# Optimization experiments

Measured on AMD Instinct MI355X. Metric: run time of the kernel, lower is better.

The kernel has to match this reference:

```python
import jax, jax.numpy as jnp
import numpy as np

B = 65536   # batch
HS = 8      # max hand size
E = 12      # card embed dim
A = 20      # max actions
KC = 4      # max cards per action (padded with 0)
NH, HD = 4, 3  # MHA heads, head dim (12/4)


def _xavier(k, out_dim, in_dim, gain):
    lim = gain * np.sqrt(6.0 / (in_dim + out_dim))
    return jax.random.uniform(k, (out_dim, in_dim), jnp.float32, -lim, lim)


def setup_inputs() -> dict:
    key = jax.random.key(0)
    ks = jax.random.split(key, 32)
    card_emb = 0.1 * jax.random.normal(ks[0], (54, E), jnp.float32)
    card_emb = card_emb.at[0].set(0.0)  # padding_idx=0
    enemy_emb = 0.1 * jax.random.normal(ks[1], (54, E), jnp.float32)
    enemy_emb = enemy_emb.at[0].set(0.0)
    inp = {
        'hand_cards': jax.random.randint(ks[2], (B, HS), 0, 54),
        'game_state': jax.random.normal(ks[3], (B, 12), jnp.float32),
        'discard_pile_cards': jax.random.uniform(ks[4], (B, 54), jnp.float32),
        'enemy_card': jax.random.randint(ks[5], (B, 1), 0, 54),
        'hand_size': jax.random.randint(ks[6], (B,), 1, HS + 1),
        'action_card_indices': jax.random.randint(ks[7], (A, KC), 0, 54),
        'num_valid_actions': 20,
        'card_emb': card_emb,
        'enemy_emb': enemy_emb,
        'in_w': _xavier(ks[8], 3 * E, E, 0.5),   # MHA in_proj (torch layout [3E,E])
        'in_b': jnp.zeros((3 * E,), jnp.float32),
        'out_w': _xavier(ks[9], E, E, 0.5),
        'out_b': jnp.zeros((E,), jnp.float32),
        'gs_w1': _xavier(ks[10], 64, 12, 0.8), 'gs_b1': jnp.zeros((64,)),
        'gs_w2': _xavier(ks[11], 6, 64, 0.8), 'gs_b2': jnp.zeros((6,)),
        'dp_w1': _xavier(ks[12], 64, 54, 0.8), 'dp_b1': jnp.zeros((64,)),
        'dp_w2': _xavier(ks[13], 6, 64, 0.8), 'dp_b2': jnp.zeros((6,)),
        'ctx_w1': _xavier(ks[14], 128, 36, 0.8), 'ctx_b1': jnp.zeros((128,)),
        'ctx_w2': _xavier(ks[15], 128, 128, 0.8), 'ctx_b2': jnp.zeros((128,)),
        'sc_w1': _xavier(ks[16], 32, 140, 0.8), 'sc_b1': jnp.zeros((32,)),
        'sc_w2': _xavier(ks[17], 1, 32, 0.8), 'sc_b2': jnp.zeros((1,)),
    }
    return inp


def reference(hand_cards, game_state, discard_pile_cards, enemy_card, hand_size,
              action_card_indices, num_valid_actions,
              card_emb, enemy_emb, in_w, in_b, out_w, out_b,
              gs_w1, gs_b1, gs_w2, gs_b2, dp_w1, dp_b1, dp_w2, dp_b2,
              ctx_w1, ctx_b1, ctx_w2, ctx_b2, sc_w1, sc_b1, sc_w2, sc_b2):
    b = hand_cards.shape[0]
    # hand embeddings + self-attention with key padding mask (card 0 = pad)
    he = card_emb[hand_cards]                                  # [B,8,12]
    mask = hand_cards != 0                                     # [B,8]
    qkv = he @ in_w.T + in_b                                   # [B,8,36]
    q, k, v = jnp.split(qkv, 3, axis=-1)
    hsplit = lambda t: t.reshape(b, HS, NH, HD)
    s = jnp.einsum('bqhd,bkhd->bhqk', hsplit(q), hsplit(k)) / np.sqrt(HD)
    s = jnp.where(mask[:, None, None, :], s, -1e9)
    attn = jax.nn.softmax(s, axis=-1)
    att = jnp.einsum('bhqk,bkhd->bqhd', attn, hsplit(v)).reshape(b, HS, E)
    att = att @ out_w.T + out_b                                # [B,8,12]
    lengths = jnp.maximum(hand_size.astype(jnp.float32), 1.0)[:, None]
    hand_ctx = att.sum(axis=1) / lengths                       # [B,12]
    # enemy / game-state / discard encoders (eval mode: dropout off)
    en = enemy_emb[enemy_card[:, 0]]                           # [B,12]
    g = jax.nn.relu(game_state @ gs_w1.T + gs_b1) @ gs_w2.T + gs_b2        # [B,6]
    d = jax.nn.relu(discard_pile_cards @ dp_w1.T + dp_b1) @ dp_w2.T + dp_b2  # [B,6]
    ctx = jnp.concatenate([hand_ctx, en, g, d], axis=-1)       # [B,36]
    ctx = jax.nn.relu(ctx @ ctx_w1.T + ctx_b1) @ ctx_w2.T + ctx_b2         # [B,128]
    # ragged per-action card lists: masked mean of card embeddings
    aemb = card_emb[action_card_indices]                       # [A,K,12]
    am = (action_card_indices != 0).astype(jnp.float32)[..., None]
    cnt = jnp.maximum(am.sum(axis=1), 1.0)
    arep = (aemb * am).sum(axis=1) / cnt                       # [A,12]
    feat = jnp.concatenate([
        jnp.broadcast_to(ctx[:, None, :], (b, A, ctx.shape[-1])),
        jnp.broadcast_to(arep[None], (b, A, E)),
    ], axis=-1)                                                # [B,A,140]
    sc = (jax.nn.relu(feat @ sc_w1.T + sc_b1) @ sc_w2.T + sc_b2)[..., 0]   # [B,A]
    valid = jnp.arange(A) < num_valid_actions
    return jnp.where(valid[None, :], sc, -1e8)
```

## Files before the change

kernel.cpp:

```cpp
#include <hip/hip_runtime.h>
#include <math.h>

#define HS 8
#define E 12
#define NA 20
#define KC 4

typedef float f32x4 __attribute__((ext_vector_type(4)));
typedef short short8 __attribute__((ext_vector_type(8)));

__device__ float g_QKVT[54 * 48];
__device__ float g_abias[NA * 32];
__device__ __align__(16) short g_dpB[2 * 4 * 64 * 16];
__device__ __align__(16) short g_ctxB[2 * 8 * 64 * 16];
__device__ __align__(16) short g_WtB[4 * 2 * 64 * 16];

__device__ __forceinline__ void split_bf16(float f, short& hi, short& lo) {
    unsigned u = __float_as_uint(f);
    unsigned r = (u + 0x7FFFu + ((u >> 16) & 1u)) >> 16;
    hi = (short)r;
    float fh = __uint_as_float(r << 16);
    unsigned v = __float_as_uint(f - fh);
    unsigned r2 = (v + 0x7FFFu + ((v >> 16) & 1u)) >> 16;
    lo = (short)r2;
}

__global__ void precompute_kernel(const float* __restrict__ card_emb,
                                  const int* __restrict__ aci,
                                  const float* __restrict__ ctx_w2,
                                  const float* __restrict__ ctx_b2,
                                  const float* __restrict__ sc_w1,
                                  const float* __restrict__ sc_b1,
                                  const float* __restrict__ in_w,
                                  const float* __restrict__ in_b,
                                  const float* __restrict__ ctx_w1,
                                  const float* __restrict__ dp_w1) {
    int t = blockIdx.x * 256 + threadIdx.x;
    if (t < 640) {
        int a = t >> 5, j = t & 31;
        float arep[E];
#pragma unroll
        for (int k2 = 0; k2 < E; ++k2) arep[k2] = 0.f;
        float cnt = 0.f;
#pragma unroll
        for (int c = 0; c < KC; ++c) {
            int idx = aci[a * KC + c];
            if (idx != 0) {
                cnt += 1.f;
#pragma unroll
                for (int k2 = 0; k2 < E; ++k2) arep[k2] += card_emb[idx * E + k2];
            }
        }
        float inv = 1.f / fmaxf(cnt, 1.f);
        float s = sc_b1[j];
#pragma unroll
        for (int k2 = 0; k2 < E; ++k2) s += sc_w1[j * 140 + 128 + k2] * (arep[k2] * inv);
        for (int i = 0; i < 128; ++i) s += sc_w1[j * 140 + i] * ctx_b2[i];
        g_abias[t] = s;
    } else if (t < 3232) {
        int t2 = t - 640;
        int c = t2 / 48, col = t2 % 48;
        int h = col / 12, s = col % 12;
        float val = 0.f;
        if (s < 9) {
            int r;
            if (s < 3) r = h * 3 + s;
            else if (s < 6) r = 12 + h * 3 + (s - 3);
            else r = 24 + h * 3 + (s - 6);
            val = in_b[r];
#pragma unroll
            for (int j = 0; j < 12; ++j) val += in_w[r * 12 + j] * card_emb[c * 12 + j];
        }
        g_QKVT[t2] = val;
    } else if (t < 7328) {
        int id = t - 3232;
        int st = id >> 9, lane = (id >> 3) & 63, j = id & 7;
        int s = st >> 2, tt = st & 3;
        int g = lane >> 4, n = lane & 15;
        int k = 32 * s + 8 * g + j, col = 16 * tt + n;
        float w = (k < 54) ? dp_w1[col * 54 + k] : 0.f;
        short hi, lo;
        split_bf16(w, hi, lo);
        int base = ((st << 6) + lane) << 4;
        g_dpB[base + j] = hi;
        g_dpB[base + 8 + j] = lo;
    } else if (t < 15520) {
        int id = t - 7328;
        int st = id >> 9, lane = (id >> 3) & 63, j = id & 7;
        int s = st >> 3, tt = st & 7;
        int g = lane >> 4, n = lane & 15;
        int k = 32 * s + 8 * g + j, col = 16 * tt + n;
        float w = (k < 36) ? ctx_w1[col * 36 + k] : 0.f;
        short hi, lo;
        split_bf16(w, hi, lo);
        int base = ((st << 6) + lane) << 4;
        g_ctxB[base + j] = hi;
        g_ctxB[base + 8 + j] = lo;
    } else if (t < 19616) {
        int id = t - 15520;
        int st = id >> 9, lane = (id >> 3) & 63, j = id & 7;
        int s = st >> 1, tt = st & 1;
        int g = lane >> 4, n = lane & 15;
        int k = 32 * s + 8 * g + j, col = 16 * tt + n;
        float w = 0.f;
        for (int i = 0; i < 128; ++i) w += sc_w1[col * 140 + i] * ctx_w2[i * 128 + k];
        short hi, lo;
        split_bf16(w, hi, lo);
        int base = ((st << 6) + lane) << 4;
        g_WtB[base + j] = hi;
        g_WtB[base + 8 + j] = lo;
    }
}

#define MFMA(a, b, c) __builtin_amdgcn_mfma_f32_16x16x32_bf16(a, b, c, 0, 0, 0)

__global__ __launch_bounds__(256) void policy_kernel(
    const int* __restrict__ hand_cards, const float* __restrict__ game_state,
    const float* __restrict__ discard, const int* __restrict__ enemy_card,
    const int* __restrict__ hand_size, const int* __restrict__ num_valid,
    const float* __restrict__ enemy_emb, const float* __restrict__ out_w,
    const float* __restrict__ out_b, const float* __restrict__ gs_w1,
    const float* __restrict__ gs_b1, const float* __restrict__ gs_w2,
    const float* __restrict__ gs_b2, const float* __restrict__ dp_w2,
    const float* __restrict__ dp_b1, const float* __restrict__ dp_b2,
    const float* __restrict__ ctx_b1, const float* __restrict__ sc_w2,
    const float* __restrict__ sc_b2, float* __restrict__ out) {
    __shared__ __align__(16) float sS[64 * 68];
    __shared__ __align__(16) float sT[4 * 16 * 36];
    __shared__ __align__(16) float sQKVT[54 * 48];
    __shared__ __align__(16) float sEN[54 * 12];
    __shared__ __align__(16) float sGS1[64 * 12];
    __shared__ __align__(16) float sGS2T[64 * 8];
    __shared__ __align__(16) float sDPW2T[64 * 12];
    __shared__ __align__(16) float sAB[NA * 36];
    __shared__ __align__(16) float sOW[144];
    __shared__ __align__(16) float sW2[32];
    __shared__ float sGSB1[64];
    __shared__ float sDPB1[64];
    __shared__ float sCB1[128];

    int tid = threadIdx.x;
    for (int i = tid; i < 54 * 48; i += 256) sQKVT[i] = g_QKVT[i];
    for (int i = tid; i < 54 * 12; i += 256) sEN[i] = enemy_emb[i];
    for (int i = tid; i < 64 * 12; i += 256) {
        int r = i / 12, c = i % 12;
        sGS1[((r & 15) * 4 + (r >> 4)) * 12 + c] = gs_w1[i];
    }
    for (int i = tid; i < 64 * 8; i += 256) {
        int r = i >> 3, c = i & 7;
        sGS2T[((r & 15) * 4 + (r >> 4)) * 8 + c] = (c < 6) ? gs_w2[c * 64 + r] : 0.f;
    }
    for (int i = tid; i < 64 * 12; i += 256) {
        int f = i / 12, c = i % 12;
        sDPW2T[i] = (c < 6) ? dp_w2[c * 64 + f] : 0.f;
    }
    for (int i = tid; i < NA * 36; i += 256) {
        int a = i / 36, c = i % 36;
        sAB[i] = (c < 32) ? g_abias[a * 32 + c] : 0.f;
    }
    if (tid < 144) sOW[tid] = out_w[tid];
    if (tid >= 160 && tid < 192) sW2[tid - 160] = sc_w2[tid - 160];
    if (tid >= 192 && tid < 256) sGSB1[tid - 192] = gs_b1[tid - 192];
    for (int i = tid; i < 64; i += 256) sDPB1[i] = dp_b1[i];
    for (int i = tid; i < 128; i += 256) sCB1[i] = ctx_b1[i];
    for (int i = tid; i < 64 * 32; i += 256) {
        int e = i >> 5, c = i & 31;
        sS[e * 68 + 36 + c] = 0.f;
    }
    __syncthreads();

    int lane = tid & 63;
    int w = tid >> 6;

    {
        int q = tid & 3;
        int el = tid >> 2;
        int b = blockIdx.x * 64 + el;
        int base = lane & ~3;

        int hc[HS];
        {
            const int4* hp = (const int4*)(hand_cards + (size_t)b * HS);
            int4 h0 = hp[0], h1 = hp[1];
            hc[0] = h0.x; hc[1] = h0.y; hc[2] = h0.z; hc[3] = h0.w;
            hc[4] = h1.x; hc[5] = h1.y; hc[6] = h1.z; hc[7] = h1.w;
        }
        int ec = enemy_card[b];

        float qk[HS][9];
#pragma unroll
        for (int p = 0; p < HS; ++p) {
            const float4* tp = (const float4*)&sQKVT[hc[p] * 48 + q * 12];
            float4 a0 = tp[0], a1 = tp[1], a2 = tp[2];
            qk[p][0] = a0.x; qk[p][1] = a0.y; qk[p][2] = a0.z;
            qk[p][3] = a0.w; qk[p][4] = a1.x; qk[p][5] = a1.y;
            qk[p][6] = a1.z; qk[p][7] = a1.w; qk[p][8] = a2.x;
        }
        const float scale = 0.5773502691896258f;
        float attv0 = 0.f, attv1 = 0.f, attv2 = 0.f;
#pragma unroll
        for (int p = 0; p < HS; ++p) {
            float s[HS];
            float mx = -3.0e38f;
#pragma unroll
            for (int k = 0; k < HS; ++k) {
                float t = (qk[p][0] * qk[k][3] + qk[p][1] * qk[k][4] + qk[p][2] * qk[k][5]) * scale;
                t = (hc[k] != 0) ? t : -1.0e9f;
                s[k] = t;
                mx = fmaxf(mx, t);
            }
            float sum = 0.f;
#pragma unroll
            for (int k = 0; k < HS; ++k) {
                float e = __expf(s[k] - mx);
                s[k] = e;
                sum += e;
            }
            float inv = 1.f / sum;
            float a0 = 0.f, a1 = 0.f, a2 = 0.f;
#pragma unroll
            for (int k = 0; k < HS; ++k) {
                a0 += s[k] * qk[k][6];
                a1 += s[k] * qk[k][7];
                a2 += s[k] * qk[k][8];
            }
            attv0 += a0 * inv; attv1 += a1 * inv; attv2 += a2 * inv;
        }
        float attw[12];
#pragma unroll
        for (int j = 0; j < 12; ++j) {
            float v = (j % 3 == 0) ? attv0 : ((j % 3 == 1) ? attv1 : attv2);
            attw[j] = __shfl(v, base + j / 3, 64);
        }
        {
            float invlen = 1.f / fmaxf((float)hand_size[b], 1.f);
#pragma unroll
            for (int t2 = 0; t2 < 3; ++t2) {
                int r = 3 * q + t2;
                float a = 8.f * out_b[r];
#pragma unroll
                for (int e = 0; e < 12; ++e) a += sOW[r * 12 + e] * attw[e];
                sS[el * 68 + r] = a * invlen;
            }
        }
#pragma unroll
        for (int t2 = 0; t2 < 3; ++t2)
            sS[el * 68 + 12 + 3 * q + t2] = sEN[ec * 12 + 3 * q + t2];

        {
            const float4* gp = (const float4*)(game_state + (size_t)b * 12);
            float4 x0 = gp[0], x1 = gp[1], x2 = gp[2];
            float acc[6] = {0.f, 0.f, 0.f, 0.f, 0.f, 0.f};
#pragma unroll 4
            for (int jj = 0; jj < 16; ++jj) {
                const float4* wr = (const float4*)&sGS1[(jj * 4 + q) * 12];
                float4 w0 = wr[0], w1 = wr[1], w2 = wr[2];
                float h = sGSB1[q * 16 + jj];
                h += w0.x * x0.x + w0.y * x0.y + w0.z * x0.z + w0.w * x0.w;
                h += w1.x * x1.x + w1.y * x1.y + w1.z * x1.z + w1.w * x1.w;
                h += w2.x * x2.x + w2.y * x2.y + w2.z * x2.z + w2.w * x2.w;
                h = fmaxf(h, 0.f);
                const float4* w2r = (const float4*)&sGS2T[(jj * 4 + q) * 8];
                float4 wa = w2r[0], wb = w2r[1];
                acc[0] += h * wa.x; acc[1] += h * wa.y; acc[2] += h * wa.z;
                acc[3] += h * wa.w; acc[4] += h * wb.x; acc[5] += h * wb.y;
            }
#pragma unroll
            for (int c = 0; c < 6; ++c) {
                float v = acc[c];
                v += __shfl_xor(v, 1, 64);
                v += __shfl_xor(v, 2, 64);
                acc[c] = v + gs_b2[c];
            }
            if (q < 3) {
                sS[el * 68 + 24 + 2 * q + 0] = acc[2 * q + 0];
                sS[el * 68 + 24 + 2 * q + 1] = acc[2 * q + 1];
            }
        }
    }

    int n = lane & 15, g = lane >> 4;
    int el2 = (w << 4) + n;
    int b2 = blockIdx.x * 64 + el2;
    {
        const float* drow = discard + (size_t)b2 * 54;
        float xa[16];
        {
            const float2* p = (const float2*)(drow + 8 * g);
            float2 v0 = p[0], v1 = p[1], v2 = p[2], v3 = p[3];
            xa[0] = v0.x; xa[1] = v0.y; xa[2] = v1.x; xa[3] = v1.y;
            xa[4] = v2.x; xa[5] = v2.y; xa[6] = v3.x; xa[7] = v3.y;
        }
#pragma unroll
        for (int j = 0; j < 8; ++j) {
            int k = 32 + 8 * g + j;
            xa[8 + j] = (k < 54) ? drow[k] : 0.f;
        }
        short8 ahi0, alo0, ahi1, alo1;
#pragma unroll
        for (int j = 0; j < 8; ++j) {
            short h, l;
            split_bf16(xa[j], h, l);     ahi0[j] = h; alo0[j] = l;
            split_bf16(xa[8 + j], h, l); ahi1[j] = h; alo1[j] = l;
        }
        f32x4 dacc[4];
#pragma unroll
        for (int t = 0; t < 4; ++t) {
            float bv = sDPB1[16 * t + n];
            f32x4 cc = {bv, bv, bv, bv};
            dacc[t] = cc;
        }
#pragma unroll
        for (int t = 0; t < 4; ++t) {
#pragma unroll
            for (int s = 0; s < 2; ++s) {
                const short8* bp = (const short8*)&g_dpB[(((s * 4 + t) << 6) + lane) << 4];
                short8 bh = bp[0], bl = bp[1];
                short8 ah = s ? ahi1 : ahi0;
                short8 al = s ? alo1 : alo0;
                dacc[t] = MFMA(ah, bh, dacc[t]);
                dacc[t] = MFMA(ah, bl, dacc[t]);
                dacc[t] = MFMA(al, bh, dacc[t]);
            }
        }
        float part[4][6];
#pragma unroll
        for (int r = 0; r < 4; ++r)
#pragma unroll
            for (int c = 0; c < 6; ++c) part[r][c] = 0.f;
#pragma unroll
        for (int t = 0; t < 4; ++t) {
            const float* wrow = &sDPW2T[(16 * t + n) * 12];
            float4 wa = *(const float4*)wrow;
            float2 wb = *(const float2*)(wrow + 4);
#pragma unroll
            for (int r = 0; r < 4; ++r) {
                float h = fmaxf(dacc[t][r], 0.f);
                part[r][0] += h * wa.x; part[r][1] += h * wa.y; part[r][2] += h * wa.z;
                part[r][3] += h * wa.w; part[r][4] += h * wb.x; part[r][5] += h * wb.y;
            }
        }
#pragma unroll
        for (int r = 0; r < 4; ++r)
#pragma unroll
            for (int c = 0; c < 6; ++c) {
                float v = part[r][c];
                v += __shfl_xor(v, 1, 64);
                v += __shfl_xor(v, 2, 64);
                v += __shfl_xor(v, 4, 64);
                v += __shfl_xor(v, 8, 64);
                part[r][c] = v;
            }
        if (n < 6) {
#pragma unroll
            for (int r = 0; r < 4; ++r) {
                float dval = part[r][0];
                dval = (n == 1) ? part[r][1] : dval;
                dval = (n == 2) ? part[r][2] : dval;
                dval = (n == 3) ? part[r][3] : dval;
                dval = (n == 4) ? part[r][4] : dval;
                dval = (n == 5) ? part[r][5] : dval;
                sS[((w << 4) + (g << 2) + r) * 68 + 30 + n] = dval + dp_b2[n];
            }
        }
    }

    asm volatile("s_waitcnt lgkmcnt(0)" ::: "memory");

    float* sTT = sT + w * 576;
    f32x4 uacc[2];
    {
        f32x4 z = {0.f, 0.f, 0.f, 0.f};
        uacc[0] = z; uacc[1] = z;
    }
    {
        const float* arow = sS + el2 * 68;
        float ca[16];
        {
            const float4* ap0 = (const float4*)(arow + 8 * g);
            float4 a0 = ap0[0], a1 = ap0[1];
            const float4* ap1 = (const float4*)(arow + 32 + 8 * g);
            float4 a2 = ap1[0], a3 = ap1[1];
            ca[0] = a0.x; ca[1] = a0.y; ca[2] = a0.z; ca[3] = a0.w;
            ca[4] = a1.x; ca[5] = a1.y; ca[6] = a1.z; ca[7] = a1.w;
            ca[8] = a2.x; ca[9] = a2.y; ca[10] = a2.z; ca[11] = a2.w;
            ca[12] = a3.x; ca[13] = a3.y; ca[14] = a3.z; ca[15] = a3.w;
        }
        short8 cahi0, calo0, cahi1, calo1;
#pragma unroll
        for (int j = 0; j < 8; ++j) {
            short h, l;
            split_bf16(ca[j], h, l);     cahi0[j] = h; calo0[j] = l;
            split_bf16(ca[8 + j], h, l); cahi1[j] = h; calo1[j] = l;
        }
#pragma unroll
        for (int p = 0; p < 4; ++p) {
            f32x4 cacc[2];
#pragma unroll
            for (int t2 = 0; t2 < 2; ++t2) {
                float bv = sCB1[(p * 2 + t2) * 16 + n];
                f32x4 cc = {bv, bv, bv, bv};
                cacc[t2] = cc;
            }
#pragma unroll
            for (int t2 = 0; t2 < 2; ++t2) {
                int tt = p * 2 + t2;
#pragma unroll
                for (int s = 0; s < 2; ++s) {
                    const short8* bp = (const short8*)&g_ctxB[(((s * 8 + tt) << 6) + lane) << 4];
                    short8 bh = bp[0], bl = bp[1];
                    short8 ah = s ? cahi1 : cahi0;
                    short8 al = s ? calo1 : calo0;
                    cacc[t2] = MFMA(ah, bh, cacc[t2]);
                    cacc[t2] = MFMA(ah, bl, cacc[t2]);
                    cacc[t2] = MFMA(al, bh, cacc[t2]);
                }
            }
#pragma unroll
            for (int t2 = 0; t2 < 2; ++t2)
#pragma unroll
                for (int r = 0; r < 4; ++r)
                    sTT[((g << 2) + r) * 36 + t2 * 16 + n] = fmaxf(cacc[t2][r], 0.f);
            asm volatile("s_waitcnt lgkmcnt(0)" ::: "memory");
            float ha[8];
            {
                const float4* hp = (const float4*)&sTT[n * 36 + 8 * g];
                float4 h0 = hp[0], h1 = hp[1];
                ha[0] = h0.x; ha[1] = h0.y; ha[2] = h0.z; ha[3] = h0.w;
                ha[4] = h1.x; ha[5] = h1.y; ha[6] = h1.z; ha[7] = h1.w;
            }
            short8 whi, wlo;
#pragma unroll
            for (int j = 0; j < 8; ++j) {
                short h, l;
                split_bf16(ha[j], h, l);
                whi[j] = h; wlo[j] = l;
            }
#pragma unroll
            for (int t2 = 0; t2 < 2; ++t2) {
                const short8* bp = (const short8*)&g_WtB[(((p * 2 + t2) << 6) + lane) << 4];
                short8 bh = bp[0], bl = bp[1];
                uacc[t2] = MFMA(whi, bh, uacc[t2]);
                uacc[t2] = MFMA(whi, bl, uacc[t2]);
                uacc[t2] = MFMA(wlo, bh, uacc[t2]);
            }
            asm volatile("s_waitcnt lgkmcnt(0)" ::: "memory");
        }
    }

    {
#pragma unroll
        for (int t2 = 0; t2 < 2; ++t2)
#pragma unroll
            for (int r = 0; r < 4; ++r)
                sTT[((g << 2) + r) * 36 + t2 * 16 + n] = uacc[t2][r];
        asm volatile("s_waitcnt lgkmcnt(0)" ::: "memory");
        float uu[32];
        {
            const float4* up = (const float4*)&sTT[n * 36];
#pragma unroll
            for (int j8 = 0; j8 < 8; ++j8) {
                float4 v = up[j8];
                uu[4 * j8 + 0] = v.x; uu[4 * j8 + 1] = v.y;
                uu[4 * j8 + 2] = v.z; uu[4 * j8 + 3] = v.w;
            }
        }
        float w2v[32];
        {
            const float4* wp = (const float4*)sW2;
#pragma unroll
            for (int j8 = 0; j8 < 8; ++j8) {
                float4 v = wp[j8];
                w2v[4 * j8 + 0] = v.x; w2v[4 * j8 + 1] = v.y;
                w2v[4 * j8 + 2] = v.z; w2v[4 * j8 + 3] = v.w;
            }
        }
        int nva = num_valid[0];
        float sb2 = sc_b2[0];
#pragma unroll
        for (int t = 0; t < 5; ++t) {
            int a = g * 5 + t;
            const float4* ab = (const float4*)&sAB[a * 36];
            float s = sb2;
#pragma unroll
            for (int j8 = 0; j8 < 8; ++j8) {
                float4 av = ab[j8];
                s += w2v[4 * j8 + 0] * fmaxf(uu[4 * j8 + 0] + av.x, 0.f);
                s += w2v[4 * j8 + 1] * fmaxf(uu[4 * j8 + 1] + av.y, 0.f);
                s += w2v[4 * j8 + 2] * fmaxf(uu[4 * j8 + 2] + av.z, 0.f);
                s += w2v[4 * j8 + 3] * fmaxf(uu[4 * j8 + 3] + av.w, 0.f);
            }
            out[(size_t)b2 * NA + a] = (a < nva) ? s : -1.0e8f;
        }
    }
}

extern "C" void kernel_launch(void* const* d_in, const int* in_sizes, int n_in,
                              void* d_out, int out_size, void* d_ws, size_t ws_size,
                              hipStream_t stream) {
    const int* hand_cards = (const int*)d_in[0];
    const float* game_state = (const float*)d_in[1];
    const float* discard = (const float*)d_in[2];
    const int* enemy_card = (const int*)d_in[3];
    const int* hand_size = (const int*)d_in[4];
    const int* aci = (const int*)d_in[5];
    const int* num_valid = (const int*)d_in[6];
    const float* card_emb = (const float*)d_in[7];
    const float* enemy_emb = (const float*)d_in[8];
    const float* in_w = (const float*)d_in[9];
    const float* in_b = (const float*)d_in[10];
    const float* out_w = (const float*)d_in[11];
    const float* out_b = (const float*)d_in[12];
    const float* gs_w1 = (const float*)d_in[13];
    const float* gs_b1 = (const float*)d_in[14];
    const float* gs_w2 = (const float*)d_in[15];
    const float* gs_b2 = (const float*)d_in[16];
    const float* dp_w1 = (const float*)d_in[17];
    const float* dp_b1 = (const float*)d_in[18];
    const float* dp_w2 = (const float*)d_in[19];
    const float* dp_b2 = (const float*)d_in[20];
    const float* ctx_w1 = (const float*)d_in[21];
    const float* ctx_b1 = (const float*)d_in[22];
    const float* ctx_w2 = (const float*)d_in[23];
    const float* ctx_b2 = (const float*)d_in[24];
    const float* sc_w1 = (const float*)d_in[25];
    const float* sc_b1 = (const float*)d_in[26];
    const float* sc_w2 = (const float*)d_in[27];
    const float* sc_b2 = (const float*)d_in[28];

    int B = in_sizes[0] / HS;

    precompute_kernel<<<77, 256, 0, stream>>>(card_emb, aci, ctx_w2, ctx_b2, sc_w1, sc_b1,
                                              in_w, in_b, ctx_w1, dp_w1);
    policy_kernel<<<B / 64, 256, 0, stream>>>(
        hand_cards, game_state, discard, enemy_card, hand_size, num_valid,
        enemy_emb, out_w, out_b, gs_w1, gs_b1, gs_w2, gs_b2, dp_w2, dp_b1, dp_b2,
        ctx_b1, sc_w2, sc_b2, (float*)d_out);
}
```

Measured before the change: 55.75 us.

## Split fused policy kernel into feature and scoring kernels via global buffer

The single fused policy kernel is split into two launches. The first computes the 36-wide context features (attention, enemy embedding, game-state and discard encoders) and writes them to a global 40-float-per-row buffer. The second reads that buffer and runs the MFMA context MLP and action scoring. This cuts per-kernel LDS use and register pressure, which may allow higher occupancy, at the cost of an extra launch and a round trip of about 10 MB through global memory.

```diff
diff --git a/kernel.cpp b/kernel.cpp
--- a/kernel.cpp
+++ b/kernel.cpp
@@ -14,6 +14,7 @@
 __device__ __align__(16) short g_dpB[2 * 4 * 64 * 16];
 __device__ __align__(16) short g_ctxB[2 * 8 * 64 * 16];
 __device__ __align__(16) short g_WtB[4 * 2 * 64 * 16];
+__device__ __align__(16) float g_c36[65536 * 40 + 64];
 
 __device__ __forceinline__ void split_bf16(float f, short& hi, short& lo) {
     unsigned u = __float_as_uint(f);
@@ -114,30 +115,23 @@
 
 #define MFMA(a, b, c) __builtin_amdgcn_mfma_f32_16x16x32_bf16(a, b, c, 0, 0, 0)
 
-__global__ __launch_bounds__(256) void policy_kernel(
+__global__ __launch_bounds__(256) void featA_kernel(
     const int* __restrict__ hand_cards, const float* __restrict__ game_state,
     const float* __restrict__ discard, const int* __restrict__ enemy_card,
-    const int* __restrict__ hand_size, const int* __restrict__ num_valid,
-    const float* __restrict__ enemy_emb, const float* __restrict__ out_w,
-    const float* __restrict__ out_b, const float* __restrict__ gs_w1,
-    const float* __restrict__ gs_b1, const float* __restrict__ gs_w2,
-    const float* __restrict__ gs_b2, const float* __restrict__ dp_w2,
-    const float* __restrict__ dp_b1, const float* __restrict__ dp_b2,
-    const float* __restrict__ ctx_b1, const float* __restrict__ sc_w2,
-    const float* __restrict__ sc_b2, float* __restrict__ out) {
-    __shared__ __align__(16) float sS[64 * 68];
-    __shared__ __align__(16) float sT[4 * 16 * 36];
+    const int* __restrict__ hand_size, const float* __restrict__ enemy_emb,
+    const float* __restrict__ out_w, const float* __restrict__ out_b,
+    const float* __restrict__ gs_w1, const float* __restrict__ gs_b1,
+    const float* __restrict__ gs_w2, const float* __restrict__ gs_b2,
+    const float* __restrict__ dp_w2, const float* __restrict__ dp_b1,
+    const float* __restrict__ dp_b2) {
     __shared__ __align__(16) float sQKVT[54 * 48];
     __shared__ __align__(16) float sEN[54 * 12];
     __shared__ __align__(16) float sGS1[64 * 12];
     __shared__ __align__(16) float sGS2T[64 * 8];
     __shared__ __align__(16) float sDPW2T[64 * 12];
-    __shared__ __align__(16) float sAB[NA * 36];
     __shared__ __align__(16) float sOW[144];
-    __shared__ __align__(16) float sW2[32];
     __shared__ float sGSB1[64];
     __shared__ float sDPB1[64];
-    __shared__ float sCB1[128];
 
     int tid = threadIdx.x;
     for (int i = tid; i < 54 * 48; i += 256) sQKVT[i] = g_QKVT[i];
@@ -154,19 +148,9 @@
         int f = i / 12, c = i % 12;
         sDPW2T[i] = (c < 6) ? dp_w2[c * 64 + f] : 0.f;
     }
-    for (int i = tid; i < NA * 36; i += 256) {
-        int a = i / 36, c = i % 36;
-        sAB[i] = (c < 32) ? g_abias[a * 32 + c] : 0.f;
-    }
     if (tid < 144) sOW[tid] = out_w[tid];
-    if (tid >= 160 && tid < 192) sW2[tid - 160] = sc_w2[tid - 160];
     if (tid >= 192 && tid < 256) sGSB1[tid - 192] = gs_b1[tid - 192];
-    for (int i = tid; i < 64; i += 256) sDPB1[i] = dp_b1[i];
-    for (int i = tid; i < 128; i += 256) sCB1[i] = ctx_b1[i];
-    for (int i = tid; i < 64 * 32; i += 256) {
-        int e = i >> 5, c = i & 31;
-        sS[e * 68 + 36 + c] = 0.f;
-    }
+    if (tid >= 128 && tid < 192) sDPB1[tid - 128] = dp_b1[tid - 128];
     __syncthreads();
 
     int lane = tid & 63;
@@ -177,6 +161,7 @@
         int el = tid >> 2;
         int b = blockIdx.x * 64 + el;
         int base = lane & ~3;
+        float* crow = g_c36 + (size_t)b * 40;
 
         int hc[HS];
         {
@@ -240,12 +225,12 @@
                 float a = 8.f * out_b[r];
 #pragma unroll
                 for (int e = 0; e < 12; ++e) a += sOW[r * 12 + e] * attw[e];
-                sS[el * 68 + r] = a * invlen;
+                crow[r] = a * invlen;
             }
         }
 #pragma unroll
         for (int t2 = 0; t2 < 3; ++t2)
-            sS[el * 68 + 12 + 3 * q + t2] = sEN[ec * 12 + 3 * q + t2];
+            crow[12 + 3 * q + t2] = sEN[ec * 12 + 3 * q + t2];
 
         {
             const float4* gp = (const float4*)(game_state + (size_t)b * 12);
@@ -273,16 +258,16 @@
                 acc[c] = v + gs_b2[c];
             }
             if (q < 3) {
-                sS[el * 68 + 24 + 2 * q + 0] = acc[2 * q + 0];
-                sS[el * 68 + 24 + 2 * q + 1] = acc[2 * q + 1];
-            }
-        }
-    }
-
-    int n = lane & 15, g = lane >> 4;
-    int el2 = (w << 4) + n;
-    int b2 = blockIdx.x * 64 + el2;
+                crow[24 + 2 * q + 0] = acc[2 * q + 0];
+                crow[24 + 2 * q + 1] = acc[2 * q + 1];
+            }
+        }
+    }
+
     {
+        int n = lane & 15, g = lane >> 4;
+        int el2 = (w << 4) + n;
+        int b2 = blockIdx.x * 64 + el2;
         const float* drow = discard + (size_t)b2 * 54;
         float xa[16];
         {
@@ -351,30 +336,56 @@
                 v += __shfl_xor(v, 8, 64);
                 part[r][c] = v;
             }
-        if (n < 6) {
+        if (n < 10) {
+            float bias = (n < 6) ? dp_b2[n] : 0.f;
 #pragma unroll
             for (int r = 0; r < 4; ++r) {
-                float dval = part[r][0];
+                float dval = 0.f;
+                dval = (n == 0) ? part[r][0] : dval;
                 dval = (n == 1) ? part[r][1] : dval;
                 dval = (n == 2) ? part[r][2] : dval;
                 dval = (n == 3) ? part[r][3] : dval;
                 dval = (n == 4) ? part[r][4] : dval;
                 dval = (n == 5) ? part[r][5] : dval;
-                sS[((w << 4) + (g << 2) + r) * 68 + 30 + n] = dval + dp_b2[n];
-            }
-        }
-    }
-
-    asm volatile("s_waitcnt lgkmcnt(0)" ::: "memory");
-
+                g_c36[(size_t)(blockIdx.x * 64 + (w << 4) + (g << 2) + r) * 40 + 30 + n] =
+                    dval + bias;
+            }
+        }
+    }
+}
+
+__global__ __launch_bounds__(256) void scoreB_kernel(
+    const int* __restrict__ num_valid, const float* __restrict__ ctx_b1,
+    const float* __restrict__ sc_w2, const float* __restrict__ sc_b2,
+    float* __restrict__ out) {
+    __shared__ __align__(16) float sT[4 * 16 * 36];
+    __shared__ __align__(16) float sAB[NA * 36];
+    __shared__ __align__(16) float sW2[32];
+    __shared__ float sCB1[128];
+
+    int tid = threadIdx.x;
+    for (int i = tid; i < NA * 36; i += 256) {
+        int a = i / 36, c = i % 36;
+        sAB[i] = (c < 32) ? g_abias[a * 32 + c] : 0.f;
+    }
+    if (tid >= 160 && tid < 192) sW2[tid - 160] = sc_w2[tid - 160];
+    if (tid < 128) sCB1[tid] = ctx_b1[tid];
+    __syncthreads();
+
+    int lane = tid & 63;
+    int w = tid >> 6;
+    int n = lane & 15, g = lane >> 4;
+    int el2 = (w << 4) + n;
+    size_t b2 = (size_t)blockIdx.x * 64 + el2;
     float* sTT = sT + w * 576;
+
     f32x4 uacc[2];
     {
         f32x4 z = {0.f, 0.f, 0.f, 0.f};
         uacc[0] = z; uacc[1] = z;
     }
     {
-        const float* arow = sS + el2 * 68;
+        const float* arow = g_c36 + b2 * 40;
         float ca[16];
         {
             const float4* ap0 = (const float4*)(arow + 8 * g);
@@ -490,7 +501,7 @@
                 s += w2v[4 * j8 + 2] * fmaxf(uu[4 * j8 + 2] + av.z, 0.f);
                 s += w2v[4 * j8 + 3] * fmaxf(uu[4 * j8 + 3] + av.w, 0.f);
             }
-            out[(size_t)b2 * NA + a] = (a < nva) ? s : -1.0e8f;
+            out[b2 * NA + a] = (a < nva) ? s : -1.0e8f;
         }
     }
 }
@@ -532,8 +543,9 @@
 
     precompute_kernel<<<77, 256, 0, stream>>>(card_emb, aci, ctx_w2, ctx_b2, sc_w1, sc_b1,
                                               in_w, in_b, ctx_w1, dp_w1);
-    policy_kernel<<<B / 64, 256, 0, stream>>>(
-        hand_cards, game_state, discard, enemy_card, hand_size, num_valid,
-        enemy_emb, out_w, out_b, gs_w1, gs_b1, gs_w2, gs_b2, dp_w2, dp_b1, dp_b2,
-        ctx_b1, sc_w2, sc_b2, (float*)d_out);
+    featA_kernel<<<B / 64, 256, 0, stream>>>(
+        hand_cards, game_state, discard, enemy_card, hand_size, enemy_emb,
+        out_w, out_b, gs_w1, gs_b1, gs_w2, gs_b2, dp_w2, dp_b1, dp_b2);
+    scoreB_kernel<<<B / 64, 256, 0, stream>>>(num_valid, ctx_b1, sc_w2, sc_b2,
+                                              (float*)d_out);
 }
```

Measured after the change: 54.58 us (median of 2 runs). -2.1%, faster.
